# Optimization experiments

Measured on AMD Instinct MI355X. Metric: run time of the kernel, lower is better.

The kernel has to match this reference:

```python
import jax, jax.numpy as jnp
import numpy as np

B, S, D = 2, 1024, 768
NH = 12
DH = D // NH
HID = 1536
G, EPG = 4, 2
E = G * EPG
TEMP = 1.0
LN_EPS = 1e-5


def setup_inputs() -> dict:
    key = jax.random.key(0)
    ks = jax.random.split(key, 8)
    s = 0.02
    return {
        "x": jax.random.normal(ks[0], (B, S, D), jnp.float32),
        "ln1_w": jnp.ones((D,), jnp.float32),
        "ln1_b": jnp.zeros((D,), jnp.float32),
        "in_proj_w": jax.random.normal(ks[1], (3 * D, D), jnp.float32) * s,
        "in_proj_b": jnp.zeros((3 * D,), jnp.float32),
        "out_proj_w": jax.random.normal(ks[2], (D, D), jnp.float32) * s,
        "out_proj_b": jnp.zeros((D,), jnp.float32),
        "ln2_w": jnp.ones((D,), jnp.float32),
        "ln2_b": jnp.zeros((D,), jnp.float32),
        "Wg": jax.random.normal(ks[3], (D, G), jnp.float32) * s,
        "bg": jnp.zeros((G,), jnp.float32),
        "We": jax.random.normal(ks[4], (G, D, EPG), jnp.float32) * s,
        "be": jnp.zeros((G, EPG), jnp.float32),
        "W1": jax.random.normal(ks[5], (E, D, HID), jnp.float32) * s,
        "b1": jnp.zeros((E, HID), jnp.float32),
        "W2": jax.random.normal(ks[6], (E, HID, D), jnp.float32) * s,
        "b2": jnp.zeros((E, D), jnp.float32),
    }


def _ln(x, w, b):
    m = x.mean(-1, keepdims=True)
    v = x.var(-1, keepdims=True)
    return (x - m) / jnp.sqrt(v + LN_EPS) * w + b


def _mha(h, wqkv, bqkv, wo, bo):
    qkv = h @ wqkv.T + bqkv                       # [B,S,3D]
    q, k, v = jnp.split(qkv, 3, axis=-1)
    q = q.reshape(B, S, NH, DH)
    k = k.reshape(B, S, NH, DH)
    v = v.reshape(B, S, NH, DH)
    scale = 1.0 / np.sqrt(DH).astype(np.float32)
    att = jnp.einsum("bqhd,bkhd->bhqk", q, k) * scale
    p = jax.nn.softmax(att, axis=-1)
    o = jnp.einsum("bhqk,bkhd->bqhd", p, v).reshape(B, S, D)
    return o @ wo.T + bo


def _moe(h, Wg, bg, We, be, W1, b1, W2, b2):
    hf = h.reshape(-1, D)                         # [N,D] tokens
    # level-1: group router (temperature softmax, top-1)
    gp = jax.nn.softmax((hf @ Wg + bg) / TEMP, axis=-1)          # [N,G]
    g = jnp.argmax(gp, axis=-1)                                   # [N]
    pg = jnp.take_along_axis(gp, g[:, None], axis=1)[:, 0]        # [N]
    # level-2: within-group expert router
    el = jnp.einsum("nd,gde->nge", hf, We) + be                   # [N,G,EPG]
    ep = jax.nn.softmax(el / TEMP, axis=-1)
    ep_g = jnp.take_along_axis(ep, g[:, None, None], axis=1)[:, 0, :]  # [N,EPG]
    e = jnp.argmax(ep_g, axis=-1)                                 # [N]
    pe = jnp.take_along_axis(ep_g, e[:, None], axis=1)[:, 0]      # [N]
    flat = g * EPG + e                                            # flat expert id [N]
    combine = jax.nn.one_hot(flat, E, dtype=hf.dtype) * (pg * pe)[:, None]  # [N,E]
    # dense expert compute (reference form of dispatch/grouped-GEMM/combine)
    hid = jax.nn.gelu(jnp.einsum("nd,edh->enh", hf, W1) + b1[:, None, :])   # [E,N,HID]
    y = jnp.einsum("enh,ehd->end", hid, W2) + b2[:, None, :]                # [E,N,D]
    out = jnp.einsum("ne,end->nd", combine, y)                              # [N,D]
    return out.reshape(h.shape)


def reference(x, ln1_w, ln1_b, in_proj_w, in_proj_b, out_proj_w, out_proj_b,
              ln2_w, ln2_b, Wg, bg, We, be, W1, b1, W2, b2):
    a = _mha(_ln(x, ln1_w, ln1_b), in_proj_w, in_proj_b, out_proj_w, out_proj_b)
    x = x + a  # dropout p=0.0 -> identity
    m = _moe(_ln(x, ln2_w, ln2_b), Wg, bg, We, be, W1, b1, W2, b2)
    return x + m
```

## Files before the change

kernel.cpp:

```cpp
#include <hip/hip_runtime.h>
#include <stdint.h>

#define B_ 2
#define S_ 1024
#define D_ 768
#define NH_ 12
#define DH_ 64
#define HID_ 1536
#define G_ 4
#define EPG_ 2
#define E_ 8
#define NTOK (B_*S_)
#define NGRP (B_*NH_*16)

typedef unsigned short u16;
typedef unsigned int u32;
typedef __bf16 bf16x8 __attribute__((ext_vector_type(8)));
typedef float f32x4 __attribute__((ext_vector_type(4)));
typedef u16 u16x4 __attribute__((ext_vector_type(4)));
typedef u32 u32x4 __attribute__((ext_vector_type(4)));

struct BfPair { u16 hi, lo; };

__device__ __forceinline__ u16 f2bf(float f){
  unsigned u = __builtin_bit_cast(unsigned, f);
  u += 0x7FFFu + ((u >> 16) & 1u);
  return (u16)(u >> 16);
}
__device__ __forceinline__ float bf2f(u16 h){
  unsigned u = ((unsigned)h) << 16;
  return __builtin_bit_cast(float, u);
}
__device__ __forceinline__ BfPair split_bf(float v){
  BfPair p;
  p.hi = f2bf(v);
  p.lo = f2bf(v - bf2f(p.hi));
  return p;
}
__device__ __forceinline__ float gelu_tanh(float x){
  float t = 0.7978845608028654f * (x + 0.044715f * x * x * x);
  float e = __expf(2.f * t);
  float th = 1.f - 2.f / (e + 1.f);
  return 0.5f * x * (1.f + th);
}
__device__ __forceinline__ void gload_lds16(const void* g, void* l){
  __builtin_amdgcn_global_load_lds(
      (const __attribute__((address_space(1))) void*)g,
      (__attribute__((address_space(3))) void*)l, 16, 0, 0);
}

__global__ __launch_bounds__(256) void k_prep(
    const float* __restrict__ in_proj_w, const float* __restrict__ out_proj_w,
    const float* __restrict__ W1, const float* __restrict__ W2,
    u16* __restrict__ inpTh, u16* __restrict__ inpTl,
    u16* __restrict__ outpTh, u16* __restrict__ outpTl,
    u16* __restrict__ W1t, u16* __restrict__ W2t){
  __shared__ float tile[32][33];
  int bid = blockIdx.x, t = threadIdx.x;
  if (bid < 2304){
    const float* src; u16 *dh, *dl; int i;
    if (bid < 1728){ src = in_proj_w; dh = inpTh; dl = inpTl; i = bid * 256 + t; }
    else           { src = out_proj_w; dh = outpTh; dl = outpTl; i = (bid - 1728) * 256 + t; }
    float4 v = ((const float4*)src)[i];
    u16x4 oh, ol;
    BfPair p0 = split_bf(v.x), p1 = split_bf(v.y), p2 = split_bf(v.z), p3 = split_bf(v.w);
    oh.x = p0.hi; ol.x = p0.lo; oh.y = p1.hi; ol.y = p1.lo;
    oh.z = p2.hi; ol.z = p2.lo; oh.w = p3.hi; ol.w = p3.lo;
    ((u16x4*)dh)[i] = oh;
    ((u16x4*)dl)[i] = ol;
  } else {
    const float* src; u16* dst; int R, C, cx, cy, e;
    if (bid < 11520){
      int r = bid - 2304; e = r / 1152; r %= 1152;
      R = D_; C = HID_; cx = r % 48; cy = r / 48;
      src = W1; dst = W1t;
    } else {
      int r = bid - 11520; e = r / 1152; r %= 1152;
      R = HID_; C = D_; cx = r % 24; cy = r / 24;
      src = W2; dst = W2t;
    }
    const float* s = src + (size_t)e * R * C;
    u16* d = dst + (size_t)e * R * C;
    int c0 = cx * 32, r0 = cy * 32;
    int tx = t & 31, ty = t >> 5;
    #pragma unroll
    for (int i = 0; i < 32; i += 8)
      tile[ty + i][tx] = s[(size_t)(r0 + ty + i) * C + c0 + tx];
    __syncthreads();
    #pragma unroll
    for (int i = 0; i < 32; i += 8)
      d[(size_t)(c0 + ty + i) * R + r0 + tx] = f2bf(tile[tx][ty + i]);
  }
}

__global__ void k_transpose_v(const u16* __restrict__ qh, const u16* __restrict__ ql,
                              u16* __restrict__ vth, u16* __restrict__ vtl){
  __shared__ u16 th[32][34], tl[32][34];
  int bh = blockIdx.z, b = bh / NH_, h = bh % NH_;
  int d0 = blockIdx.x * 32, s0 = blockIdx.y * 32;
  #pragma unroll
  for (int i = 0; i < 32; i += 8){
    size_t src = (size_t)(b * S_ + s0 + threadIdx.y + i) * (3 * D_) + 2 * D_ + h * DH_ + d0 + threadIdx.x;
    th[threadIdx.y + i][threadIdx.x] = qh[src];
    tl[threadIdx.y + i][threadIdx.x] = ql[src];
  }
  __syncthreads();
  #pragma unroll
  for (int i = 0; i < 32; i += 8){
    size_t dst = ((size_t)bh * DH_ + d0 + threadIdx.y + i) * S_ + s0 + threadIdx.x;
    vth[dst] = th[threadIdx.x][threadIdx.y + i];
    vtl[dst] = tl[threadIdx.x][threadIdx.y + i];
  }
}

__global__ __launch_bounds__(256) void k_layernorm(
    const float* __restrict__ x, const float* __restrict__ w, const float* __restrict__ b,
    u16* __restrict__ oh, u16* __restrict__ ol, float* __restrict__ of){
  int row = blockIdx.x;
  const float* xr = x + (size_t)row * D_;
  int t = threadIdx.x;
  float v0 = xr[t], v1 = xr[t + 256], v2 = xr[t + 512];
  float s = v0 + v1 + v2;
  float sq = v0 * v0 + v1 * v1 + v2 * v2;
  #pragma unroll
  for (int m = 1; m < 64; m <<= 1){ s += __shfl_xor(s, m); sq += __shfl_xor(sq, m); }
  __shared__ float ls[4], lq[4];
  int wid = t >> 6;
  if ((t & 63) == 0){ ls[wid] = s; lq[wid] = sq; }
  __syncthreads();
  s = ls[0] + ls[1] + ls[2] + ls[3];
  sq = lq[0] + lq[1] + lq[2] + lq[3];
  float mean = s * (1.f / D_);
  float var = sq * (1.f / D_) - mean * mean;
  float rstd = rsqrtf(var + 1e-5f);
  #pragma unroll
  for (int i = 0; i < 3; i++){
    int dcol = t + i * 256;
    float v = (i == 0 ? v0 : (i == 1 ? v1 : v2));
    float y = (v - mean) * rstd * w[dcol] + b[dcol];
    BfPair p = split_bf(y);
    oh[(size_t)row * D_ + dcol] = p.hi;
    if (ol) ol[(size_t)row * D_ + dcol] = p.lo;
    if (of) of[(size_t)row * D_ + dcol] = y;
  }
}

template<int EPI>
__global__ __launch_bounds__(256) void k_gemm3(
    const u16* __restrict__ Ah, const u16* __restrict__ Al,
    const u16* __restrict__ Bh, const u16* __restrict__ Bl,
    const float* __restrict__ bias, const float* __restrict__ resid,
    u16* __restrict__ outh, u16* __restrict__ outl, float* __restrict__ outf,
    int M, int N, int K){
  __shared__ alignas(16) u16 Ash[2][128 * 32];
  __shared__ alignas(16) u16 Asl[2][128 * 32];
  __shared__ alignas(16) u16 Bsh[2][64 * 32];
  __shared__ alignas(16) u16 Bsl[2][64 * 32];
  int m0 = blockIdx.x * 128, n0 = blockIdx.y * 64;
  int tid = threadIdx.x, w = tid >> 6, l = tid & 63;
  f32x4 acc[2][4];
  #pragma unroll
  for (int i = 0; i < 2; i++)
    #pragma unroll
    for (int j = 0; j < 4; j++) acc[i][j] = f32x4{0.f, 0.f, 0.f, 0.f};
  int srow = l >> 2;
  int scol = 8 * ((l & 3) ^ ((l >> 2) & 3));
  const u16* gAh0 = Ah + (size_t)(m0 + w * 32 + srow) * K + scol;
  const u16* gAh1 = gAh0 + (size_t)16 * K;
  const u16* gAl0 = Al + (size_t)(m0 + w * 32 + srow) * K + scol;
  const u16* gAl1 = gAl0 + (size_t)16 * K;
  const u16* gBh = Bh + (size_t)(n0 + w * 16 + srow) * K + scol;
  const u16* gBl = Bl + (size_t)(n0 + w * 16 + srow) * K + scol;
  int dA0 = (w * 32) * 32, dA1 = (w * 32 + 16) * 32, dB = (w * 16) * 32;
  auto STAGE = [&](int buf, int k0){
    gload_lds16(gAh0 + k0, &Ash[buf][dA0]);
    gload_lds16(gAh1 + k0, &Ash[buf][dA1]);
    gload_lds16(gAl0 + k0, &Asl[buf][dA0]);
    gload_lds16(gAl1 + k0, &Asl[buf][dA1]);
    gload_lds16(gBh + k0, &Bsh[buf][dB]);
    gload_lds16(gBl + k0, &Bsl[buf][dB]);
  };
  STAGE(0, 0);
  __syncthreads();
  int nk = K / 32;
  int ca = (l >> 4) ^ (l & 3);
  int ai0 = (w * 32 + (l & 15)) * 32 + 8 * ca;
  int ai1 = ai0 + 16 * 32;
  for (int t = 0; t < nk; t++){
    int cur = t & 1;
    if (t + 1 < nk) STAGE(cur ^ 1, (t + 1) * 32);
    bf16x8 afh[2], afl[2], bfh[4], bfl[4];
    afh[0] = *(const bf16x8*)&Ash[cur][ai0];
    afh[1] = *(const bf16x8*)&Ash[cur][ai1];
    afl[0] = *(const bf16x8*)&Asl[cur][ai0];
    afl[1] = *(const bf16x8*)&Asl[cur][ai1];
    #pragma unroll
    for (int ni = 0; ni < 4; ni++){
      int bi = (ni * 16 + (l & 15)) * 32 + 8 * ca;
      bfh[ni] = *(const bf16x8*)&Bsh[cur][bi];
      bfl[ni] = *(const bf16x8*)&Bsl[cur][bi];
    }
    #pragma unroll
    for (int mi = 0; mi < 2; mi++)
      #pragma unroll
      for (int ni = 0; ni < 4; ni++){
        acc[mi][ni] = __builtin_amdgcn_mfma_f32_16x16x32_bf16(afh[mi], bfh[ni], acc[mi][ni], 0, 0, 0);
        acc[mi][ni] = __builtin_amdgcn_mfma_f32_16x16x32_bf16(afh[mi], bfl[ni], acc[mi][ni], 0, 0, 0);
        acc[mi][ni] = __builtin_amdgcn_mfma_f32_16x16x32_bf16(afl[mi], bfh[ni], acc[mi][ni], 0, 0, 0);
      }
    __syncthreads();
  }
  int r4 = (l >> 4) * 4, cc = l & 15;
  #pragma unroll
  for (int mi = 0; mi < 2; mi++){
    #pragma unroll
    for (int ni = 0; ni < 4; ni++){
      int col = n0 + ni * 16 + cc;
      float bv = bias ? bias[col] : 0.f;
      #pragma unroll
      for (int r = 0; r < 4; r++){
        int row = m0 + w * 32 + mi * 16 + r4 + r;
        float v = acc[mi][ni][r] + bv;
        if (EPI == 0){
          BfPair p = split_bf(v);
          outh[(size_t)row * N + col] = p.hi;
          outl[(size_t)row * N + col] = p.lo;
        } else {
          outf[(size_t)row * N + col] = v + resid[(size_t)row * N + col];
        }
      }
    }
  }
}

__global__ __launch_bounds__(256) void k_attn3(
    const u16* __restrict__ qkvh, const u16* __restrict__ qkvl,
    const u16* __restrict__ vth, const u16* __restrict__ vtl,
    float* __restrict__ po0, float* __restrict__ po1,
    float* __restrict__ pm, float* __restrict__ plsum){
  __shared__ alignas(16) u16 Ksh[2][32 * 64];
  __shared__ alignas(16) u16 Ksl[2][32 * 64];
  __shared__ alignas(16) u16 Vsh[2][64 * 32];
  __shared__ alignas(16) u16 Vsl[2][64 * 32];
  int bh = blockIdx.x, qb = blockIdx.y, ks = blockIdx.z;
  int b = bh / NH_, h = bh % NH_;
  int g = bh * 16 + qb;
  int tid = threadIdx.x, w = tid >> 6, l = tid & 63;
  int q0 = qb * 64 + w * 16;
  const int RS = 3 * D_;
  size_t qoff = (size_t)(b * S_ + q0 + (l & 15)) * RS + h * DH_ + 8 * (l >> 4);
  bf16x8 aqh[2], aql[2];
  aqh[0] = *(const bf16x8*)(qkvh + qoff); aqh[1] = *(const bf16x8*)(qkvh + qoff + 32);
  aql[0] = *(const bf16x8*)(qkvl + qoff); aql[1] = *(const bf16x8*)(qkvl + qoff + 32);
  f32x4 oacc[4];
  #pragma unroll
  for (int i = 0; i < 4; i++) oacc[i] = f32x4{0.f, 0.f, 0.f, 0.f};
  float mrun = -1e30f, lrun = 0.f;

  size_t koff = (size_t)(b * S_ + w * 8 + (l >> 3)) * RS + D_ + h * DH_ + 8 * ((l & 7) ^ (l >> 3));
  const u16* Kgh = qkvh + koff;
  const u16* Kgl = qkvl + koff;
  size_t voff = ((size_t)bh * DH_ + w * 16 + (l >> 2)) * S_ + 8 * ((l & 3) ^ ((l >> 2) & 3));
  const u16* Vgh = vth + voff;
  const u16* Vgl = vtl + voff;
  int wdst = w * 512;

  auto STAGE = [&](int buf, int akt){
    gload_lds16(Kgh + (size_t)(akt * 32) * RS, &Ksh[buf][wdst]);
    gload_lds16(Kgl + (size_t)(akt * 32) * RS, &Ksl[buf][wdst]);
    gload_lds16(Vgh + akt * 32, &Vsh[buf][wdst]);
    gload_lds16(Vgl + akt * 32, &Vsl[buf][wdst]);
  };
  int kt0 = ks * 16;
  STAGE(0, kt0);
  __syncthreads();

  int ck0 = (l >> 4) ^ (l & 7);
  int ck1 = ck0 ^ 4;
  int cv = (l >> 4) ^ (l & 3);
  int s1 = (l & 15) | ((l & 16) << 1);
  int s2 = s1 + 16;
  bool up = (l & 32) != 0;

  for (int kt = 0; kt < 16; kt++){
    int cur = kt & 1;
    if (kt + 1 < 16) STAGE(cur ^ 1, kt0 + kt + 1);
    f32x4 st[2];
    #pragma unroll
    for (int nt = 0; nt < 2; nt++){
      int rbase = (nt * 16 + (l & 15)) * 64;
      bf16x8 kh0 = *(const bf16x8*)&Ksh[cur][rbase + 8 * ck0];
      bf16x8 kh1 = *(const bf16x8*)&Ksh[cur][rbase + 8 * ck1];
      bf16x8 kl0 = *(const bf16x8*)&Ksl[cur][rbase + 8 * ck0];
      bf16x8 kl1 = *(const bf16x8*)&Ksl[cur][rbase + 8 * ck1];
      f32x4 c = f32x4{0.f, 0.f, 0.f, 0.f};
      c = __builtin_amdgcn_mfma_f32_16x16x32_bf16(kh0, aqh[0], c, 0, 0, 0);
      c = __builtin_amdgcn_mfma_f32_16x16x32_bf16(kh1, aqh[1], c, 0, 0, 0);
      c = __builtin_amdgcn_mfma_f32_16x16x32_bf16(kh0, aql[0], c, 0, 0, 0);
      c = __builtin_amdgcn_mfma_f32_16x16x32_bf16(kh1, aql[1], c, 0, 0, 0);
      c = __builtin_amdgcn_mfma_f32_16x16x32_bf16(kl0, aqh[0], c, 0, 0, 0);
      c = __builtin_amdgcn_mfma_f32_16x16x32_bf16(kl1, aqh[1], c, 0, 0, 0);
      st[nt] = c;
    }
    float mx = fmaxf(fmaxf(fmaxf(st[0][0], st[0][1]), fmaxf(st[0][2], st[0][3])),
                     fmaxf(fmaxf(st[1][0], st[1][1]), fmaxf(st[1][2], st[1][3])));
    mx = fmaxf(mx, __shfl_xor(mx, 16));
    mx = fmaxf(mx, __shfl_xor(mx, 32));
    mx *= 0.125f;
    if (!__all(mx <= mrun)){
      float mnew = fmaxf(mrun, mx);
      float alpha = __expf(mrun - mnew);
      lrun *= alpha;
      #pragma unroll
      for (int r = 0; r < 4; r++){
        float ar = __shfl(alpha, (l & 48) | (((l >> 4) << 2) + r));
        oacc[0][r] *= ar; oacc[1][r] *= ar; oacc[2][r] *= ar; oacc[3][r] *= ar;
      }
      mrun = mnew;
    }
    float p[8]; float sum = 0.f;
    #pragma unroll
    for (int j = 0; j < 8; j++){
      p[j] = __expf(st[j >> 2][j & 3] * 0.125f - mrun);
      sum += p[j];
    }
    sum += __shfl_xor(sum, 16);
    sum += __shfl_xor(sum, 32);
    lrun += sum;
    u32 pkh[4], pkl[4];
    #pragma unroll
    for (int i = 0; i < 4; i++){
      BfPair a = split_bf(p[2 * i]), bb = split_bf(p[2 * i + 1]);
      pkh[i] = (u32)a.hi | ((u32)bb.hi << 16);
      pkl[i] = (u32)a.lo | ((u32)bb.lo << 16);
    }
    u32 ah0 = __shfl((int)pkh[0], s1), ah1 = __shfl((int)pkh[1], s1);
    u32 ah2 = __shfl((int)pkh[2], s1), ah3 = __shfl((int)pkh[3], s1);
    u32 bh0 = __shfl((int)pkh[0], s2), bh1 = __shfl((int)pkh[1], s2);
    u32 bh2 = __shfl((int)pkh[2], s2), bh3 = __shfl((int)pkh[3], s2);
    u32 al0 = __shfl((int)pkl[0], s1), al1 = __shfl((int)pkl[1], s1);
    u32 al2 = __shfl((int)pkl[2], s1), al3 = __shfl((int)pkl[3], s1);
    u32 bl0 = __shfl((int)pkl[0], s2), bl1 = __shfl((int)pkl[1], s2);
    u32 bl2 = __shfl((int)pkl[2], s2), bl3 = __shfl((int)pkl[3], s2);
    u32x4 fh, fl;
    fh.x = up ? ah2 : ah0; fh.y = up ? ah3 : ah1; fh.z = up ? bh2 : bh0; fh.w = up ? bh3 : bh1;
    fl.x = up ? al2 : al0; fl.y = up ? al3 : al1; fl.z = up ? bl2 : bl0; fl.w = up ? bl3 : bl1;
    bf16x8 pa_h = __builtin_bit_cast(bf16x8, fh);
    bf16x8 pa_l = __builtin_bit_cast(bf16x8, fl);
    #pragma unroll
    for (int dt = 0; dt < 4; dt++){
      int vb = (dt * 16 + (l & 15)) * 32 + 8 * cv;
      bf16x8 bvh = *(const bf16x8*)&Vsh[cur][vb];
      bf16x8 bvl = *(const bf16x8*)&Vsl[cur][vb];
      oacc[dt] = __builtin_amdgcn_mfma_f32_16x16x32_bf16(pa_h, bvh, oacc[dt], 0, 0, 0);
      oacc[dt] = __builtin_amdgcn_mfma_f32_16x16x32_bf16(pa_h, bvl, oacc[dt], 0, 0, 0);
      oacc[dt] = __builtin_amdgcn_mfma_f32_16x16x32_bf16(pa_l, bvh, oacc[dt], 0, 0, 0);
    }
    __syncthreads();
  }
  float* po = ks ? po1 : po0;
  #pragma unroll
  for (int dt = 0; dt < 4; dt++)
    #pragma unroll
    for (int r = 0; r < 4; r++){
      int qloc = w * 16 + (l >> 4) * 4 + r;
      int d = dt * 16 + (l & 15);
      po[((size_t)(g * 64 + qloc)) * 64 + d] = oacc[dt][r];
    }
  if (l < 16){
    pm[(ks * NGRP + g) * 64 + w * 16 + l] = mrun;
    plsum[(ks * NGRP + g) * 64 + w * 16 + l] = lrun;
  }
}

__global__ __launch_bounds__(256) void k_attn_merge(
    const float* __restrict__ po0, const float* __restrict__ po1,
    const float* __restrict__ pm, const float* __restrict__ plsum,
    u16* __restrict__ oh, u16* __restrict__ ol){
  int bh = blockIdx.x, qb = blockIdx.y;
  int b = bh / NH_, h = bh % NH_;
  int g = bh * 16 + qb;
  int t = threadIdx.x;
  int q = t >> 2, d0 = (t & 3) * 16;
  float m0 = pm[g * 64 + q],      m1 = pm[NGRP * 64 + g * 64 + q];
  float l0 = plsum[g * 64 + q],   l1 = plsum[NGRP * 64 + g * 64 + q];
  float M = fmaxf(m0, m1);
  float a0 = __expf(m0 - M), a1 = __expf(m1 - M);
  float rcp = 1.f / (l0 * a0 + l1 * a1);
  size_t base = ((size_t)(g * 64 + q)) * 64 + d0;
  size_t orow = (size_t)(b * S_ + qb * 64 + q) * D_ + h * DH_ + d0;
  #pragma unroll
  for (int j = 0; j < 16; j++){
    float v = (po0[base + j] * a0 + po1[base + j] * a1) * rcp;
    BfPair p = split_bf(v);
    oh[orow + j] = p.hi;
    ol[orow + j] = p.lo;
  }
}

__global__ __launch_bounds__(256) void k_router(
    const float* __restrict__ h2f, const float* __restrict__ Wg, const float* __restrict__ bg,
    const float* __restrict__ We, const float* __restrict__ be,
    int* __restrict__ flat, float* __restrict__ pc){
  int w = threadIdx.x >> 6, l = threadIdx.x & 63;
  int n = blockIdx.x * 4 + w;
  const float* hr = h2f + (size_t)n * D_;
  float pl[4] = {0.f, 0.f, 0.f, 0.f};
  for (int d = l; d < D_; d += 64){
    float hv = hr[d];
    float4 wg = *(const float4*)&Wg[d * 4];
    pl[0] += hv * wg.x; pl[1] += hv * wg.y; pl[2] += hv * wg.z; pl[3] += hv * wg.w;
  }
  #pragma unroll
  for (int m = 1; m < 64; m <<= 1)
    #pragma unroll
    for (int g = 0; g < 4; g++) pl[g] += __shfl_xor(pl[g], m);
  float lg[4];
  #pragma unroll
  for (int g = 0; g < 4; g++) lg[g] = pl[g] + bg[g];
  int gi = 0; float gm = lg[0];
  #pragma unroll
  for (int g = 1; g < 4; g++) if (lg[g] > gm){ gm = lg[g]; gi = g; }
  float gs = 0.f;
  #pragma unroll
  for (int g = 0; g < 4; g++) gs += expf(lg[g] - gm);
  float pg = 1.f / gs;
  float e0 = 0.f, e1 = 0.f;
  for (int d = l; d < D_; d += 64){
    float hv = hr[d];
    float2 we = *(const float2*)&We[((size_t)gi * D_ + d) * 2];
    e0 += hv * we.x; e1 += hv * we.y;
  }
  #pragma unroll
  for (int m = 1; m < 64; m <<= 1){ e0 += __shfl_xor(e0, m); e1 += __shfl_xor(e1, m); }
  e0 += be[gi * 2]; e1 += be[gi * 2 + 1];
  int ei; float pe;
  if (e1 > e0){ ei = 1; pe = 1.f / (1.f + expf(e0 - e1)); }
  else        { ei = 0; pe = 1.f / (1.f + expf(e1 - e0)); }
  if (l == 0){
    flat[n] = gi * 2 + ei;
    pc[n] = pg * pe;
  }
}

__global__ __launch_bounds__(1024) void k_bucket(
    const int* __restrict__ flat, int* __restrict__ moeI, int* __restrict__ order){
  __shared__ int cnt[E_], off[E_], cur[E_];
  int t = threadIdx.x;
  if (t < E_){ cnt[t] = 0; cur[t] = 0; }
  __syncthreads();
  int n0 = t, n1 = t + 1024;
  int f0 = flat[n0], f1 = flat[n1];
  atomicAdd(&cnt[f0], 1);
  atomicAdd(&cnt[f1], 1);
  __syncthreads();
  if (t == 0){
    int s = 0;
    for (int e = 0; e < E_; e++){
      off[e] = s; moeI[16 + e] = s; moeI[e] = cnt[e]; s += cnt[e];
    }
  }
  __syncthreads();
  int p0 = atomicAdd(&cur[f0], 1);
  order[off[f0] + p0] = n0;
  int p1 = atomicAdd(&cur[f1], 1);
  order[off[f1] + p1] = n1;
}

__global__ __launch_bounds__(256) void k_moe_gemm1(
    const u16* __restrict__ h2, const u16* __restrict__ W1t, const float* __restrict__ b1,
    const int* __restrict__ order, const int* __restrict__ moeI, u16* __restrict__ hid){
  int e = blockIdx.x, mt = blockIdx.y, nt = blockIdx.z;
  int cnt = moeI[e];
  if (mt * 64 >= cnt) return;
  int off = moeI[16 + e];
  __shared__ alignas(16) u16 As[2][64 * 64];
  __shared__ alignas(16) u16 Bs[2][64 * 64];
  int tid = threadIdx.x, w = tid >> 6, l = tid & 63;
  int wr = w >> 1, wc = w & 1;
  f32x4 acc[2][2];
  #pragma unroll
  for (int i = 0; i < 2; i++)
    #pragma unroll
    for (int j = 0; j < 2; j++) acc[i][j] = f32x4{0.f, 0.f, 0.f, 0.f};
  int r0 = w * 16 + (l >> 3);
  int sch = 8 * ((l & 7) ^ (l >> 3));
  int tokA0 = order[off + min(mt * 64 + r0, cnt - 1)];
  int tokA1 = order[off + min(mt * 64 + r0 + 8, cnt - 1)];
  const u16* gA0 = h2 + (size_t)tokA0 * D_ + sch;
  const u16* gA1 = h2 + (size_t)tokA1 * D_ + sch;
  const u16* gB0 = W1t + (size_t)e * HID_ * D_ + (size_t)(nt * 64 + r0) * D_ + sch;
  const u16* gB1 = gB0 + (size_t)8 * D_;
  int d0 = (w * 16) * 64, d1 = (w * 16 + 8) * 64;
  auto STAGE = [&](int buf, int k0){
    gload_lds16(gA0 + k0, &As[buf][d0]);
    gload_lds16(gA1 + k0, &As[buf][d1]);
    gload_lds16(gB0 + k0, &Bs[buf][d0]);
    gload_lds16(gB1 + k0, &Bs[buf][d1]);
  };
  STAGE(0, 0);
  __syncthreads();
  int c0 = (l >> 4) ^ (l & 7);
  int c1 = ((l >> 4) + 4) ^ (l & 7);
  const int nk = D_ / 64;
  for (int t = 0; t < nk; t++){
    int cur = t & 1;
    if (t + 1 < nk) STAGE(cur ^ 1, (t + 1) * 64);
    bf16x8 af[2][2], bfr[2][2];
    #pragma unroll
    for (int mi = 0; mi < 2; mi++){
      int rbase = (wr * 32 + mi * 16 + (l & 15)) * 64;
      af[mi][0] = *(const bf16x8*)&As[cur][rbase + 8 * c0];
      af[mi][1] = *(const bf16x8*)&As[cur][rbase + 8 * c1];
    }
    #pragma unroll
    for (int ni = 0; ni < 2; ni++){
      int rbase = (wc * 32 + ni * 16 + (l & 15)) * 64;
      bfr[ni][0] = *(const bf16x8*)&Bs[cur][rbase + 8 * c0];
      bfr[ni][1] = *(const bf16x8*)&Bs[cur][rbase + 8 * c1];
    }
    #pragma unroll
    for (int mi = 0; mi < 2; mi++)
      #pragma unroll
      for (int ni = 0; ni < 2; ni++){
        acc[mi][ni] = __builtin_amdgcn_mfma_f32_16x16x32_bf16(af[mi][0], bfr[ni][0], acc[mi][ni], 0, 0, 0);
        acc[mi][ni] = __builtin_amdgcn_mfma_f32_16x16x32_bf16(af[mi][1], bfr[ni][1], acc[mi][ni], 0, 0, 0);
      }
    __syncthreads();
  }
  int r4 = (l >> 4) * 4, cc = l & 15;
  #pragma unroll
  for (int mi = 0; mi < 2; mi++){
    #pragma unroll
    for (int ni = 0; ni < 2; ni++){
      int col = nt * 64 + wc * 32 + ni * 16 + cc;
      float bv = b1[e * HID_ + col];
      #pragma unroll
      for (int r = 0; r < 4; r++){
        int rowl = mt * 64 + wr * 32 + mi * 16 + r4 + r;
        if (rowl < cnt){
          float v = gelu_tanh(acc[mi][ni][r] + bv);
          hid[(size_t)(off + rowl) * HID_ + col] = f2bf(v);
        }
      }
    }
  }
}

__global__ __launch_bounds__(256) void k_moe_gemm2(
    const u16* __restrict__ hid, const u16* __restrict__ W2t, const float* __restrict__ b2,
    const int* __restrict__ order, const int* __restrict__ moeI,
    const float* __restrict__ pc, const float* __restrict__ x2, float* __restrict__ out){
  int e = blockIdx.x, mt = blockIdx.y, nt = blockIdx.z;
  int cnt = moeI[e];
  if (mt * 64 >= cnt) return;
  int off = moeI[16 + e];
  __shared__ alignas(16) u16 As[2][64 * 64];
  __shared__ alignas(16) u16 Bs[2][64 * 64];
  int tid = threadIdx.x, w = tid >> 6, l = tid & 63;
  int wr = w >> 1, wc = w & 1;
  f32x4 acc[2][2];
  #pragma unroll
  for (int i = 0; i < 2; i++)
    #pragma unroll
    for (int j = 0; j < 2; j++) acc[i][j] = f32x4{0.f, 0.f, 0.f, 0.f};
  int r0 = w * 16 + (l >> 3);
  int sch = 8 * ((l & 7) ^ (l >> 3));
  int ar0 = off + min(mt * 64 + r0, cnt - 1);
  int ar1 = off + min(mt * 64 + r0 + 8, cnt - 1);
  const u16* gA0 = hid + (size_t)ar0 * HID_ + sch;
  const u16* gA1 = hid + (size_t)ar1 * HID_ + sch;
  const u16* gB0 = W2t + (size_t)e * D_ * HID_ + (size_t)(nt * 64 + r0) * HID_ + sch;
  const u16* gB1 = gB0 + (size_t)8 * HID_;
  int d0 = (w * 16) * 64, d1 = (w * 16 + 8) * 64;
  auto STAGE = [&](int buf, int k0){
    gload_lds16(gA0 + k0, &As[buf][d0]);
    gload_lds16(gA1 + k0, &As[buf][d1]);
    gload_lds16(gB0 + k0, &Bs[buf][d0]);
    gload_lds16(gB1 + k0, &Bs[buf][d1]);
  };
  STAGE(0, 0);
  __syncthreads();
  int c0 = (l >> 4) ^ (l & 7);
  int c1 = ((l >> 4) + 4) ^ (l & 7);
  const int nk = HID_ / 64;
  for (int t = 0; t < nk; t++){
    int cur = t & 1;
    if (t + 1 < nk) STAGE(cur ^ 1, (t + 1) * 64);
    bf16x8 af[2][2], bfr[2][2];
    #pragma unroll
    for (int mi = 0; mi < 2; mi++){
      int rbase = (wr * 32 + mi * 16 + (l & 15)) * 64;
      af[mi][0] = *(const bf16x8*)&As[cur][rbase + 8 * c0];
      af[mi][1] = *(const bf16x8*)&As[cur][rbase + 8 * c1];
    }
    #pragma unroll
    for (int ni = 0; ni < 2; ni++){
      int rbase = (wc * 32 + ni * 16 + (l & 15)) * 64;
      bfr[ni][0] = *(const bf16x8*)&Bs[cur][rbase + 8 * c0];
      bfr[ni][1] = *(const bf16x8*)&Bs[cur][rbase + 8 * c1];
    }
    #pragma unroll
    for (int mi = 0; mi < 2; mi++)
      #pragma unroll
      for (int ni = 0; ni < 2; ni++){
        acc[mi][ni] = __builtin_amdgcn_mfma_f32_16x16x32_bf16(af[mi][0], bfr[ni][0], acc[mi][ni], 0, 0, 0);
        acc[mi][ni] = __builtin_amdgcn_mfma_f32_16x16x32_bf16(af[mi][1], bfr[ni][1], acc[mi][ni], 0, 0, 0);
      }
    __syncthreads();
  }
  int r4 = (l >> 4) * 4, cc = l & 15;
  #pragma unroll
  for (int mi = 0; mi < 2; mi++){
    #pragma unroll
    for (int r = 0; r < 4; r++){
      int rowl = mt * 64 + wr * 32 + mi * 16 + r4 + r;
      if (rowl < cnt){
        int tok = order[off + rowl];
        float pv = pc[tok];
        #pragma unroll
        for (int ni = 0; ni < 2; ni++){
          int col = nt * 64 + wc * 32 + ni * 16 + cc;
          float v = acc[mi][ni][r] + b2[e * D_ + col];
          out[(size_t)tok * D_ + col] = x2[(size_t)tok * D_ + col] + pv * v;
        }
      }
    }
  }
}

extern "C" void kernel_launch(void* const* d_in, const int* in_sizes, int n_in,
                              void* d_out, int out_size, void* d_ws, size_t ws_size,
                              hipStream_t stream){
  const float* x         = (const float*)d_in[0];
  const float* ln1_w     = (const float*)d_in[1];
  const float* ln1_b     = (const float*)d_in[2];
  const float* in_proj_w = (const float*)d_in[3];
  const float* in_proj_b = (const float*)d_in[4];
  const float* out_proj_w= (const float*)d_in[5];
  const float* out_proj_b= (const float*)d_in[6];
  const float* ln2_w     = (const float*)d_in[7];
  const float* ln2_b     = (const float*)d_in[8];
  const float* Wg        = (const float*)d_in[9];
  const float* bg        = (const float*)d_in[10];
  const float* We        = (const float*)d_in[11];
  const float* be        = (const float*)d_in[12];
  const float* W1        = (const float*)d_in[13];
  const float* b1        = (const float*)d_in[14];
  const float* W2        = (const float*)d_in[15];
  const float* b2        = (const float*)d_in[16];
  float* out = (float*)d_out;

  char* ws = (char*)d_ws;
  size_t off = 0;
  auto alloc = [&](size_t bytes) -> char* {
    char* p = ws + off;
    off += (bytes + 255) & ~(size_t)255;
    return p;
  };
  u16*   inpTh = (u16*)  alloc((size_t)3 * D_ * D_ * 2);
  u16*   inpTl = (u16*)  alloc((size_t)3 * D_ * D_ * 2);
  u16*   outpTh= (u16*)  alloc((size_t)D_ * D_ * 2);
  u16*   outpTl= (u16*)  alloc((size_t)D_ * D_ * 2);
  u16*   W1t  = (u16*)  alloc((size_t)E_ * HID_ * D_ * 2);
  u16*   W2t  = (u16*)  alloc((size_t)E_ * D_ * HID_ * 2);
  u16*   qkvh = (u16*)  alloc((size_t)NTOK * 3 * D_ * 2);
  u16*   qkvl = (u16*)  alloc((size_t)NTOK * 3 * D_ * 2);
  u16*   h1h  = (u16*)  alloc((size_t)NTOK * D_ * 2);
  u16*   h1l  = (u16*)  alloc((size_t)NTOK * D_ * 2);
  u16*   vth  = (u16*)  alloc((size_t)B_ * NH_ * DH_ * S_ * 2);
  u16*   vtl  = (u16*)  alloc((size_t)B_ * NH_ * DH_ * S_ * 2);
  float* x2   = (float*)alloc((size_t)NTOK * D_ * 4);
  u16*   h2   = (u16*)  alloc((size_t)NTOK * D_ * 2);
  int*   flat = (int*)  alloc(NTOK * 4);
  float* pc   = (float*)alloc(NTOK * 4);
  int*   order= (int*)  alloc(NTOK * 4);
  int*   moeI = (int*)  alloc(32 * 4);
  float* po0  = (float*)h1h;
  float* po1  = (float*)inpTh;
  float* pmArr= (float*)((char*)inpTh + 6291456);
  float* plArr= (float*)((char*)inpTh + 6291456 + 196608);
  u16*   attnh= qkvh;
  u16*   attnl= qkvl;
  float* h2f  = (float*)qkvh;
  u16*   hid  = (u16*)qkvl;

  k_prep<<<dim3(20736), dim3(256), 0, stream>>>(
      in_proj_w, out_proj_w, W1, W2, inpTh, inpTl, outpTh, outpTl, W1t, W2t);
  k_layernorm<<<dim3(NTOK), dim3(256), 0, stream>>>(x, ln1_w, ln1_b, h1h, h1l, (float*)nullptr);
  k_gemm3<0><<<dim3(NTOK / 128, 3 * D_ / 64), dim3(256), 0, stream>>>(
      h1h, h1l, inpTh, inpTl, in_proj_b, nullptr, qkvh, qkvl, nullptr, NTOK, 3 * D_, D_);
  k_transpose_v<<<dim3(DH_ / 32, S_ / 32, B_ * NH_), dim3(32, 8), 0, stream>>>(qkvh, qkvl, vth, vtl);
  k_attn3<<<dim3(B_ * NH_, S_ / 64, 2), dim3(256), 0, stream>>>(
      qkvh, qkvl, vth, vtl, po0, po1, pmArr, plArr);
  k_attn_merge<<<dim3(B_ * NH_, S_ / 64), dim3(256), 0, stream>>>(
      po0, po1, pmArr, plArr, attnh, attnl);
  k_gemm3<1><<<dim3(NTOK / 128, D_ / 64), dim3(256), 0, stream>>>(
      attnh, attnl, outpTh, outpTl, out_proj_b, x, nullptr, nullptr, x2, NTOK, D_, D_);
  k_layernorm<<<dim3(NTOK), dim3(256), 0, stream>>>(x2, ln2_w, ln2_b, h2, (u16*)nullptr, h2f);
  k_router<<<dim3(NTOK / 4), dim3(256), 0, stream>>>(h2f, Wg, bg, We, be, flat, pc);
  k_bucket<<<dim3(1), dim3(1024), 0, stream>>>(flat, moeI, order);
  k_moe_gemm1<<<dim3(E_, NTOK / 64, HID_ / 64), dim3(256), 0, stream>>>(h2, W1t, b1, order, moeI, hid);
  k_moe_gemm2<<<dim3(E_, NTOK / 64, D_ / 64), dim3(256), 0, stream>>>(hid, W2t, b2, order, moeI, pc, x2, out);
}
```

Baseline: 209.7 us.

## Fuse V transpose into QKV GEMM epilogue and split attention keys three ways

After: 207.7 us. Within noise of the previous version (-1.0%).

```diff
diff --git a/kernel.cpp b/kernel.cpp
--- a/kernel.cpp
+++ b/kernel.cpp
@@ -12,12 +12,14 @@
 #define E_ 8
 #define NTOK (B_*S_)
 #define NGRP (B_*NH_*16)
+#define KSPLIT 3
 
 typedef unsigned short u16;
 typedef unsigned int u32;
 typedef __bf16 bf16x8 __attribute__((ext_vector_type(8)));
 typedef float f32x4 __attribute__((ext_vector_type(4)));
 typedef u16 u16x4 __attribute__((ext_vector_type(4)));
+typedef u16 u16x8 __attribute__((ext_vector_type(8)));
 typedef u32 u32x4 __attribute__((ext_vector_type(4)));
 
 struct BfPair { u16 hi, lo; };
@@ -93,26 +95,6 @@
   }
 }
 
-__global__ void k_transpose_v(const u16* __restrict__ qh, const u16* __restrict__ ql,
-                              u16* __restrict__ vth, u16* __restrict__ vtl){
-  __shared__ u16 th[32][34], tl[32][34];
-  int bh = blockIdx.z, b = bh / NH_, h = bh % NH_;
-  int d0 = blockIdx.x * 32, s0 = blockIdx.y * 32;
-  #pragma unroll
-  for (int i = 0; i < 32; i += 8){
-    size_t src = (size_t)(b * S_ + s0 + threadIdx.y + i) * (3 * D_) + 2 * D_ + h * DH_ + d0 + threadIdx.x;
-    th[threadIdx.y + i][threadIdx.x] = qh[src];
-    tl[threadIdx.y + i][threadIdx.x] = ql[src];
-  }
-  __syncthreads();
-  #pragma unroll
-  for (int i = 0; i < 32; i += 8){
-    size_t dst = ((size_t)bh * DH_ + d0 + threadIdx.y + i) * S_ + s0 + threadIdx.x;
-    vth[dst] = th[threadIdx.x][threadIdx.y + i];
-    vtl[dst] = tl[threadIdx.x][threadIdx.y + i];
-  }
-}
-
 __global__ __launch_bounds__(256) void k_layernorm(
     const float* __restrict__ x, const float* __restrict__ w, const float* __restrict__ b,
     u16* __restrict__ oh, u16* __restrict__ ol, float* __restrict__ of){
@@ -151,6 +133,7 @@
     const u16* __restrict__ Bh, const u16* __restrict__ Bl,
     const float* __restrict__ bias, const float* __restrict__ resid,
     u16* __restrict__ outh, u16* __restrict__ outl, float* __restrict__ outf,
+    u16* __restrict__ vth, u16* __restrict__ vtl,
     int M, int N, int K){
   __shared__ alignas(16) u16 Ash[2][128 * 32];
   __shared__ alignas(16) u16 Asl[2][128 * 32];
@@ -211,6 +194,39 @@
     __syncthreads();
   }
   int r4 = (l >> 4) * 4, cc = l & 15;
+  if (EPI == 0 && n0 >= 2 * D_){
+    int hh = (n0 - 2 * D_) >> 6;
+    int bb = m0 / S_;
+    int bhl = bb * NH_ + hh;
+    int sg0 = m0 % S_;
+    u16* VhL = (u16*)&Ash[0][0];
+    u16* VlL = (u16*)&Asl[0][0];
+    #pragma unroll
+    for (int mi = 0; mi < 2; mi++){
+      #pragma unroll
+      for (int ni = 0; ni < 4; ni++){
+        int d = ni * 16 + cc;
+        float bv = bias ? bias[n0 + d] : 0.f;
+        int sl = w * 32 + mi * 16 + r4;
+        u16x4 h4, l4;
+        #pragma unroll
+        for (int r = 0; r < 4; r++){
+          BfPair p = split_bf(acc[mi][ni][r] + bv);
+          h4[r] = p.hi; l4[r] = p.lo;
+        }
+        *(u16x4*)&VhL[d * 128 + sl] = h4;
+        *(u16x4*)&VlL[d * 128 + sl] = l4;
+      }
+    }
+    __syncthreads();
+    for (int i = tid; i < 64 * 16; i += 256){
+      int d = i >> 4, s8 = (i & 15) * 8;
+      size_t go = ((size_t)bhl * DH_ + d) * S_ + sg0 + s8;
+      *(u16x8*)&vth[go] = *(const u16x8*)&VhL[d * 128 + s8];
+      *(u16x8*)&vtl[go] = *(const u16x8*)&VlL[d * 128 + s8];
+    }
+    return;
+  }
   #pragma unroll
   for (int mi = 0; mi < 2; mi++){
     #pragma unroll
@@ -236,7 +252,7 @@
 __global__ __launch_bounds__(256) void k_attn3(
     const u16* __restrict__ qkvh, const u16* __restrict__ qkvl,
     const u16* __restrict__ vth, const u16* __restrict__ vtl,
-    float* __restrict__ po0, float* __restrict__ po1,
+    float* __restrict__ po0, float* __restrict__ po1, float* __restrict__ po2,
     float* __restrict__ pm, float* __restrict__ plsum){
   __shared__ alignas(16) u16 Ksh[2][32 * 64];
   __shared__ alignas(16) u16 Ksl[2][32 * 64];
@@ -271,7 +287,8 @@
     gload_lds16(Vgh + akt * 32, &Vsh[buf][wdst]);
     gload_lds16(Vgl + akt * 32, &Vsl[buf][wdst]);
   };
-  int kt0 = ks * 16;
+  int kt0 = (ks * 32) / KSPLIT;
+  int ktE = ((ks + 1) * 32) / KSPLIT;
   STAGE(0, kt0);
   __syncthreads();
 
@@ -282,9 +299,9 @@
   int s2 = s1 + 16;
   bool up = (l & 32) != 0;
 
-  for (int kt = 0; kt < 16; kt++){
-    int cur = kt & 1;
-    if (kt + 1 < 16) STAGE(cur ^ 1, kt0 + kt + 1);
+  for (int kt = kt0; kt < ktE; kt++){
+    int cur = (kt - kt0) & 1;
+    if (kt + 1 < ktE) STAGE(cur ^ 1, kt + 1);
     f32x4 st[2];
     #pragma unroll
     for (int nt = 0; nt < 2; nt++){
@@ -358,7 +375,7 @@
     }
     __syncthreads();
   }
-  float* po = ks ? po1 : po0;
+  float* po = (ks == 0) ? po0 : ((ks == 1) ? po1 : po2);
   #pragma unroll
   for (int dt = 0; dt < 4; dt++)
     #pragma unroll
@@ -374,7 +391,7 @@
 }
 
 __global__ __launch_bounds__(256) void k_attn_merge(
-    const float* __restrict__ po0, const float* __restrict__ po1,
+    const float* __restrict__ po0, const float* __restrict__ po1, const float* __restrict__ po2,
     const float* __restrict__ pm, const float* __restrict__ plsum,
     u16* __restrict__ oh, u16* __restrict__ ol){
   int bh = blockIdx.x, qb = blockIdx.y;
@@ -382,16 +399,20 @@
   int g = bh * 16 + qb;
   int t = threadIdx.x;
   int q = t >> 2, d0 = (t & 3) * 16;
-  float m0 = pm[g * 64 + q],      m1 = pm[NGRP * 64 + g * 64 + q];
-  float l0 = plsum[g * 64 + q],   l1 = plsum[NGRP * 64 + g * 64 + q];
-  float M = fmaxf(m0, m1);
-  float a0 = __expf(m0 - M), a1 = __expf(m1 - M);
-  float rcp = 1.f / (l0 * a0 + l1 * a1);
+  float m0 = pm[g * 64 + q];
+  float m1 = pm[(NGRP + g) * 64 + q];
+  float m2 = pm[(2 * NGRP + g) * 64 + q];
+  float l0 = plsum[g * 64 + q];
+  float l1 = plsum[(NGRP + g) * 64 + q];
+  float l2 = plsum[(2 * NGRP + g) * 64 + q];
+  float M = fmaxf(fmaxf(m0, m1), m2);
+  float a0 = __expf(m0 - M), a1 = __expf(m1 - M), a2 = __expf(m2 - M);
+  float rcp = 1.f / (l0 * a0 + l1 * a1 + l2 * a2);
   size_t base = ((size_t)(g * 64 + q)) * 64 + d0;
   size_t orow = (size_t)(b * S_ + qb * 64 + q) * D_ + h * DH_ + d0;
   #pragma unroll
   for (int j = 0; j < 16; j++){
-    float v = (po0[base + j] * a0 + po1[base + j] * a1) * rcp;
+    float v = (po0[base + j] * a0 + po1[base + j] * a1 + po2[base + j] * a2) * rcp;
     BfPair p = split_bf(v);
     oh[orow + j] = p.hi;
     ol[orow + j] = p.lo;
@@ -678,8 +699,9 @@
   int*   moeI = (int*)  alloc(32 * 4);
   float* po0  = (float*)h1h;
   float* po1  = (float*)inpTh;
+  float* po2  = x2;
   float* pmArr= (float*)((char*)inpTh + 6291456);
-  float* plArr= (float*)((char*)inpTh + 6291456 + 196608);
+  float* plArr= (float*)((char*)inpTh + 6291456 + 294912);
   u16*   attnh= qkvh;
   u16*   attnl= qkvl;
   float* h2f  = (float*)qkvh;
@@ -689,14 +711,14 @@
       in_proj_w, out_proj_w, W1, W2, inpTh, inpTl, outpTh, outpTl, W1t, W2t);
   k_layernorm<<<dim3(NTOK), dim3(256), 0, stream>>>(x, ln1_w, ln1_b, h1h, h1l, (float*)nullptr);
   k_gemm3<0><<<dim3(NTOK / 128, 3 * D_ / 64), dim3(256), 0, stream>>>(
-      h1h, h1l, inpTh, inpTl, in_proj_b, nullptr, qkvh, qkvl, nullptr, NTOK, 3 * D_, D_);
-  k_transpose_v<<<dim3(DH_ / 32, S_ / 32, B_ * NH_), dim3(32, 8), 0, stream>>>(qkvh, qkvl, vth, vtl);
-  k_attn3<<<dim3(B_ * NH_, S_ / 64, 2), dim3(256), 0, stream>>>(
-      qkvh, qkvl, vth, vtl, po0, po1, pmArr, plArr);
+      h1h, h1l, inpTh, inpTl, in_proj_b, nullptr, qkvh, qkvl, nullptr, vth, vtl, NTOK, 3 * D_, D_);
+  k_attn3<<<dim3(B_ * NH_, S_ / 64, KSPLIT), dim3(256), 0, stream>>>(
+      qkvh, qkvl, vth, vtl, po0, po1, po2, pmArr, plArr);
   k_attn_merge<<<dim3(B_ * NH_, S_ / 64), dim3(256), 0, stream>>>(
-      po0, po1, pmArr, plArr, attnh, attnl);
+      po0, po1, po2, pmArr, plArr, attnh, attnl);
   k_gemm3<1><<<dim3(NTOK / 128, D_ / 64), dim3(256), 0, stream>>>(
-      attnh, attnl, outpTh, outpTl, out_proj_b, x, nullptr, nullptr, x2, NTOK, D_, D_);
+      attnh, attnl, outpTh, outpTl, out_proj_b, x, nullptr, nullptr, x2,
+      (u16*)nullptr, (u16*)nullptr, NTOK, D_, D_);
   k_layernorm<<<dim3(NTOK), dim3(256), 0, stream>>>(x2, ln2_w, ln2_b, h2, (u16*)nullptr, h2f);
   k_router<<<dim3(NTOK / 4), dim3(256), 0, stream>>>(h2f, Wg, bg, We, be, flat, pc);
   k_bucket<<<dim3(1), dim3(1024), 0, stream>>>(flat, moeI, order);
```
